# Kernel optimization log

Measured on AMD Instinct MI355X. Metric: run time of the kernel, lower is better.

## Reference

```python
import jax, jax.numpy as jnp
import numpy as np
from jax import lax

EPS = 1e-12

def _l2norm(x):
    # F.normalize(x, dim=-1): x / max(||x||, eps)
    n = jnp.sqrt(jnp.sum(x * x, axis=-1, keepdims=True))
    return x / jnp.maximum(n, EPS)

def _knn_edges(z, k):
    """k nearest neighbors (excluding self) via squared euclidean distance.
    Squared distance preserves the top-k ordering of torch.cdist."""
    N = z.shape[0]
    sq = jnp.sum(z * z, axis=1)                        # [N]
    d2 = sq[:, None] + sq[None, :] - 2.0 * (z @ z.T)   # [N, N]
    _, idx = lax.top_k(-d2, k + 1)                     # nearest first; col 0 is self
    tgt = idx[:, 1:].reshape(-1)                       # [N*k]
    src = jnp.repeat(jnp.arange(N, dtype=idx.dtype), k)
    return src, tgt

def _count_components(A):
    """Connected components on dense boolean adjacency A [N,N] via
    min-label propagation with pointer jumping (jit-friendly BFS replacement)."""
    N = A.shape[0]
    labels0 = jnp.arange(N, dtype=jnp.int32)

    def cond(state):
        return state[1]

    def body(state):
        labels, _ = state
        # min label over neighbors (N as sentinel where no edge)
        nbr_min = jnp.min(jnp.where(A, labels[None, :], jnp.int32(N)), axis=1)
        new = jnp.minimum(labels, nbr_min)
        new = new[new]  # pointer jumping: label of my label
        return new, jnp.any(new != labels)

    labels, _ = lax.while_loop(cond, body, (labels0, jnp.array(True)))
    # a node whose final label equals its own index is the component minimum
    return jnp.sum(labels == jnp.arange(N, dtype=jnp.int32))

def _level(feats, W, ratio):
    N = feats.shape[0]
    z = _l2norm(feats @ W.T)                 # Linear(bias=False) then normalize
    k = max(3, int(ratio * N))               # static python int
    k = min(k, N - 1)
    src, tgt = _knn_edges(z, k)
    A = jnp.zeros((N, N), dtype=bool)
    A = A.at[src, tgt].set(True).at[tgt, src].set(True)   # symmetrize
    comps = _count_components(lax.stop_gradient(A))
    num_edges = N * k                                     # src.numel() in torch code
    b0 = comps
    b1 = jnp.maximum(0, num_edges - N + comps)
    return b0, b1

RATIOS = (0.1, 0.05)

def setup_inputs() -> dict:
    key = jax.random.key(0)
    k1, k2, k3 = jax.random.split(key, 3)
    N, C = 4096, 512
    feats = jax.random.normal(k1, (N, C), dtype=jnp.float32)
    W0 = jax.random.normal(k2, (512, C), dtype=jnp.float32) / np.sqrt(C)
    W1 = jax.random.normal(k3, (256, C), dtype=jnp.float32) / np.sqrt(C)
    return {"feats": feats, "W0": W0, "W1": W1}

def reference(feats, W0, W1):
    b0_0, b1_0 = _level(feats, W0, RATIOS[0])
    b0_1, b1_1 = _level(feats, W1, RATIOS[1])
    return jnp.stack([b0_0 + b0_1, b1_0 + b1_1]).astype(jnp.float32)
```

## Files before the change

kernel.cpp:

```cpp
#include <hip/hip_runtime.h>
#include <hip/hip_bf16.h>

#define NPTS   4096
#define ADJ_W  128

typedef __attribute__((ext_vector_type(8))) short short8;
typedef __attribute__((ext_vector_type(8))) unsigned short u16x8;
typedef __attribute__((ext_vector_type(4))) unsigned short u16x4;
typedef __attribute__((ext_vector_type(16))) unsigned char u8x16;
typedef __attribute__((ext_vector_type(4))) float f32x4;
typedef __attribute__((ext_vector_type(4))) int i32x4;
typedef __attribute__((ext_vector_type(4))) unsigned u32x4;

__device__ __forceinline__ unsigned short bf16_bits(float x) {
  __hip_bfloat16 h = __float2bfloat16(x);
  return __builtin_bit_cast(unsigned short, h);
}

__device__ __forceinline__ unsigned char quant8(float f) {
  return (unsigned char)(int)fminf(fmaxf((f + 0.25f) * 512.0f, 0.0f), 255.0f);
}

__device__ __forceinline__ void async16(const void* g, void* l) {
  __builtin_amdgcn_global_load_lds(
      (const __attribute__((address_space(1))) void*)g,
      (__attribute__((address_space(3))) void*)l, 16, 0, 0);
}

__global__ __launch_bounds__(256) void convert_all(
    const float* __restrict__ feats, const float* __restrict__ W0,
    const float* __restrict__ W1, unsigned short* __restrict__ fh,
    unsigned short* __restrict__ wcat) {
  const int NF = 4096 * 512 / 4, NW0 = 512 * 512 / 4, NW1 = 256 * 512 / 4;
  for (int u = blockIdx.x * 256 + threadIdx.x; u < NF + NW0 + NW1;
       u += gridDim.x * 256) {
    const float* src;
    unsigned short* dst;
    int idx;
    if (u < NF)            { src = feats; dst = fh;   idx = u; }
    else if (u < NF + NW0) { src = W0;    dst = wcat; idx = u - NF; }
    else                   { src = W1;    dst = wcat + NW0 * 4; idx = u - NF - NW0; }
    f32x4 v = *(const f32x4*)(src + (size_t)idx * 4);
    u16x4 o;
    #pragma unroll
    for (int e = 0; e < 4; e++) o[e] = bf16_bits(v[e]);
    *(u16x4*)(dst + (size_t)idx * 4) = o;
  }
}

__global__ __launch_bounds__(256) void gemm_bt_f32(
    const __hip_bfloat16* __restrict__ A, const __hip_bfloat16* __restrict__ B,
    float* __restrict__ C, int M, int N, int K) {
  __shared__ __attribute__((aligned(16))) __hip_bfloat16 As[2][128 * 32];
  __shared__ __attribute__((aligned(16))) __hip_bfloat16 Bs[2][128 * 32];
  int tid = threadIdx.x;
  int lane = tid & 63, wave = tid >> 6;
  int wr = wave >> 1, wc = wave & 1;
  int row0 = blockIdx.y * 128, col0 = blockIdx.x * 128;

  f32x4 acc[4][4] = {};
  int r = lane & 15, kh = lane >> 4;

  auto stage = [&](int buf, int k0) {
    #pragma unroll
    for (int q = 0; q < 2; q++) {
      int chunk = q * 256 + tid;
      int row = chunk >> 2;
      int cb = chunk & 3;
      async16(&A[(size_t)(row0 + row) * K + k0 + cb * 8],
              &As[buf][(q * 256 + wave * 64) * 8]);
      async16(&B[(size_t)(col0 + row) * K + k0 + cb * 8],
              &Bs[buf][(q * 256 + wave * 64) * 8]);
    }
  };

  int nt = K >> 5;
  stage(0, 0);
  int cur = 0;
  for (int t = 0; t < nt; t++) {
    if (t + 1 < nt) {
      stage(cur ^ 1, (t + 1) * 32);
      asm volatile("s_waitcnt vmcnt(4)" ::: "memory");
    } else {
      asm volatile("s_waitcnt vmcnt(0)" ::: "memory");
    }
    __builtin_amdgcn_s_barrier();
    __builtin_amdgcn_sched_barrier(0);

    short8 a[4], b[4];
    #pragma unroll
    for (int mi = 0; mi < 4; mi++)
      a[mi] = *(short8*)(&As[cur][(wr * 64 + mi * 16 + r) * 32 + kh * 8]);
    #pragma unroll
    for (int ni = 0; ni < 4; ni++)
      b[ni] = *(short8*)(&Bs[cur][(wc * 64 + ni * 16 + r) * 32 + kh * 8]);
    #pragma unroll
    for (int mi = 0; mi < 4; mi++)
      #pragma unroll
      for (int ni = 0; ni < 4; ni++)
        acc[mi][ni] = __builtin_amdgcn_mfma_f32_16x16x32_bf16(a[mi], b[ni], acc[mi][ni], 0, 0, 0);
    __builtin_amdgcn_s_barrier();
    cur ^= 1;
  }

  int rq = lane >> 4;
  #pragma unroll
  for (int mi = 0; mi < 4; mi++)
    #pragma unroll
    for (int ni = 0; ni < 4; ni++)
      #pragma unroll
      for (int j = 0; j < 4; j++) {
        int rr = row0 + wr * 64 + mi * 16 + rq * 4 + j;
        int cc = col0 + wc * 64 + ni * 16 + r;
        C[(size_t)rr * N + cc] = acc[mi][ni][j];
      }
}

__global__ __launch_bounds__(512) void gemm_s_tri(
    const __hip_bfloat16* __restrict__ Z0, const __hip_bfloat16* __restrict__ Z1,
    unsigned char* __restrict__ S0, unsigned char* __restrict__ S1) {
  __shared__ __attribute__((aligned(16))) __hip_bfloat16 As[2][128 * 32];
  __shared__ __attribute__((aligned(16))) __hip_bfloat16 Bs[2][128 * 32];
  unsigned char* Cs = (unsigned char*)As;

  int b = blockIdx.x;
  int s = (b & 7) * 132 + (b >> 3);
  int lvl = s & 1;
  int t = s >> 1;
  int I = (int)((sqrtf(8.0f * (float)t + 1.0f) - 1.0f) * 0.5f);
  if (t - I * (I + 1) / 2 > I) I++;
  int J = t - I * (I + 1) / 2;

  const __hip_bfloat16* Z = lvl ? Z1 : Z0;
  unsigned char* S = lvl ? S1 : S0;
  int K = lvl ? 256 : 512;
  int row0 = I * 128, col0 = J * 128;

  int tid = threadIdx.x;
  int lane = tid & 63, wave = tid >> 6;
  int wr = wave >> 2, wc = wave & 3;

  f32x4 acc[4][2] = {};
  int r = lane & 15, kh = lane >> 4, rq = lane >> 4;

  auto stage = [&](int buf, int k0) {
    int row = tid >> 2;
    int cb = tid & 3;
    async16(&Z[(size_t)(row0 + row) * K + k0 + cb * 8],
            &As[buf][(wave * 64) * 8]);
    async16(&Z[(size_t)(col0 + row) * K + k0 + cb * 8],
            &Bs[buf][(wave * 64) * 8]);
  };

  int nt = K >> 5;
  stage(0, 0);
  int cur = 0;
  for (int tt = 0; tt < nt; tt++) {
    if (tt + 1 < nt) {
      stage(cur ^ 1, (tt + 1) * 32);
      asm volatile("s_waitcnt vmcnt(2)" ::: "memory");
    } else {
      asm volatile("s_waitcnt vmcnt(0)" ::: "memory");
    }
    __builtin_amdgcn_s_barrier();
    __builtin_amdgcn_sched_barrier(0);

    short8 a[4], bfr[2];
    #pragma unroll
    for (int mi = 0; mi < 4; mi++)
      a[mi] = *(short8*)(&As[cur][(wr * 64 + mi * 16 + r) * 32 + kh * 8]);
    #pragma unroll
    for (int ni = 0; ni < 2; ni++)
      bfr[ni] = *(short8*)(&Bs[cur][(wc * 32 + ni * 16 + r) * 32 + kh * 8]);
    #pragma unroll
    for (int mi = 0; mi < 4; mi++)
      #pragma unroll
      for (int ni = 0; ni < 2; ni++)
        acc[mi][ni] = __builtin_amdgcn_mfma_f32_16x16x32_bf16(a[mi], bfr[ni], acc[mi][ni], 0, 0, 0);
    __builtin_amdgcn_s_barrier();
    cur ^= 1;
  }
  __syncthreads();

  int erow = tid >> 4;
  int ecol = (tid & 15) * 8;

  #pragma unroll
  for (int s4 = 0; s4 < 4; s4++) {
    if (wr == (s4 >> 1)) {
      const int half = s4 & 1;
      #pragma unroll
      for (int mi_l = 0; mi_l < 2; mi_l++) {
        const int mi = half * 2 + mi_l;
        #pragma unroll
        for (int ni = 0; ni < 2; ni++) {
          int lrow0 = mi * 16 + rq * 4 - half * 32;
          int cc = wc * 32 + ni * 16 + r;
          #pragma unroll
          for (int j = 0; j < 4; j++)
            Cs[(lrow0 + j) * 144 + cc] = quant8(acc[mi][ni][j]);
        }
      }
    }
    __syncthreads();
    {
      unsigned long long v = *(const unsigned long long*)(&Cs[erow * 144 + ecol]);
      *(unsigned long long*)(&S[(size_t)(row0 + s4 * 32 + erow) * NPTS + col0 + ecol]) = v;
    }
    __syncthreads();
  }

  if (I != J) {
    #pragma unroll
    for (int s4 = 0; s4 < 4; s4++) {
      if (wc == s4) {
        #pragma unroll
        for (int ni = 0; ni < 2; ni++) {
          int lrow = ni * 16 + r;
          #pragma unroll
          for (int mi = 0; mi < 4; mi++) {
            int rr = wr * 64 + mi * 16 + rq * 4;
            unsigned v = (unsigned)quant8(acc[mi][ni][0])
                       | ((unsigned)quant8(acc[mi][ni][1]) << 8)
                       | ((unsigned)quant8(acc[mi][ni][2]) << 16)
                       | ((unsigned)quant8(acc[mi][ni][3]) << 24);
            *(unsigned*)(&Cs[lrow * 144 + rr]) = v;
          }
        }
      }
      __syncthreads();
      {
        unsigned long long v = *(const unsigned long long*)(&Cs[erow * 144 + ecol]);
        *(unsigned long long*)(&S[(size_t)(col0 + s4 * 32 + erow) * NPTS + row0 + ecol]) = v;
      }
      __syncthreads();
    }
  }
}

__global__ __launch_bounds__(64) void l2norm_fused(const float* __restrict__ Zcat,
                                                   unsigned short* __restrict__ Z0h,
                                                   unsigned short* __restrict__ Z1h) {
  int bid = blockIdx.x;
  int lvl = bid >> 12, row = bid & 4095;
  int D = lvl ? 256 : 512;
  const float* src = Zcat + (size_t)row * 768 + (lvl ? 512 : 0);
  unsigned short* dst = lvl ? (Z1h + (size_t)row * 256) : (Z0h + (size_t)row * 512);
  int d4 = D >> 2;
  int lane = threadIdx.x;
  float ss = 0.f;
  for (int j = lane; j < d4; j += 64) {
    f32x4 v = *(const f32x4*)(src + j * 4);
    ss += v[0] * v[0] + v[1] * v[1] + v[2] * v[2] + v[3] * v[3];
  }
  #pragma unroll
  for (int off = 32; off; off >>= 1) ss += __shfl_xor(ss, off);
  float inv = 1.0f / fmaxf(sqrtf(ss), 1e-12f);
  for (int j = lane; j < d4; j += 64) {
    f32x4 v = *(const f32x4*)(src + j * 4);
    u16x4 o;
    #pragma unroll
    for (int e = 0; e < 4; e++) o[e] = bf16_bits(v[e] * inv);
    *(u16x4*)(dst + j * 4) = o;
  }
}

__global__ __launch_bounds__(256) void select_mark_f(
    const unsigned char* __restrict__ S0, const unsigned char* __restrict__ S1,
    unsigned* __restrict__ adjR) {
  __shared__ int hist[4][256];
  __shared__ int sfx[257];
  __shared__ int wtot[4];
  __shared__ unsigned rowbits[ADJ_W];
  __shared__ int sh_b;
  int bid = blockIdx.x;
  int lvl = bid >> 12, i = bid & 4095;
  int k = lvl ? 204 : 409;
  const unsigned char* row = (lvl ? S1 : S0) + (size_t)i * NPTS;
  unsigned* adj = adjR + ((size_t)lvl * NPTS + i) * ADJ_W;
  int tid = threadIdx.x;
  int lane = tid & 63, wid = tid >> 6;
  int target = k + 1;

  #pragma unroll
  for (int w = 0; w < 4; w++) hist[w][tid] = 0;
  if (tid < ADJ_W) rowbits[tid] = 0;
  __syncthreads();

  u8x16 v = *(const u8x16*)(row + tid * 16);
  #pragma unroll
  for (int e = 0; e < 16; e++)
    atomicAdd(&hist[wid][v[e]], 1);
  __syncthreads();

  {
    int c = hist[0][tid] + hist[1][tid] + hist[2][tid] + hist[3][tid];
    int sv = c;
    #pragma unroll
    for (int off = 1; off < 64; off <<= 1) {
      int u = __shfl_down(sv, off);
      if (lane + off < 64) sv += u;
    }
    if (lane == 0) wtot[wid] = sv;
    __syncthreads();
    int add = 0;
    for (int w = wid + 1; w < 4; w++) add += wtot[w];
    sfx[tid] = sv + add;
    if (tid == 0) sfx[256] = 0;
  }
  __syncthreads();
  if (sfx[tid] >= target && sfx[tid + 1] < target) sh_b = tid;
  __syncthreads();
  int bq = sh_b;

  #pragma unroll
  for (int e = 0; e < 16; e++) {
    int j = tid * 16 + e;
    if ((int)v[e] >= bq) atomicOr(&rowbits[j >> 5], 1u << (j & 31));
  }
  __syncthreads();
  if (tid == 0) rowbits[i >> 5] &= ~(1u << (i & 31));
  __syncthreads();
  if (tid < ADJ_W) adj[tid] = rowbits[tid];
}

__global__ __launch_bounds__(256) void sym_or_f(const unsigned* __restrict__ adjR,
                                                unsigned* __restrict__ adjS) {
  int bid = blockIdx.x;
  int lvl = bid >> 11;
  size_t base = (size_t)lvl * NPTS * ADJ_W;
  int tid = threadIdx.x;
  int lane = tid & 63, wave = tid >> 6;
  int half = lane >> 5, l = lane & 31;
  int tile = (bid & 2047) * 8 + wave * 2 + half;
  int I = tile >> 7, J = tile & 127;
  unsigned y = adjR[base + (size_t)(J * 32 + l) * ADJ_W + I];
  #pragma unroll
  for (int j = 16; j; j >>= 1) {
    unsigned m = 0xFFFFFFFFu / ((1u << j) + 1u);
    unsigned t = __shfl_xor(y, j);
    y = ((l & j) == 0) ? ((y & m) | ((t & m) << j))
                       : ((y & ~m) | ((t >> j) & m));
  }
  size_t d = base + (size_t)(I * 32 + l) * ADJ_W + J;
  adjS[d] = adjR[d] | y;
}

__global__ __launch_bounds__(256) void sweep0_f(const unsigned* __restrict__ adjS,
                                                int* __restrict__ labels) {
  int gi = blockIdx.x * 256 + threadIdx.x;
  int lvl = gi >> 12, node = gi & 4095;
  const unsigned* row = adjS + ((size_t)lvl * NPTS + node) * ADJ_W;
  int m = node;
  for (int w = 0; w < ADJ_W; w += 4) {
    u32x4 v = *(const u32x4*)(row + w);
    if (v[0]) { m = min(m, (w + 0) * 32 + __ffs(v[0]) - 1); break; }
    if (v[1]) { m = min(m, (w + 1) * 32 + __ffs(v[1]) - 1); break; }
    if (v[2]) { m = min(m, (w + 2) * 32 + __ffs(v[2]) - 1); break; }
    if (v[3]) { m = min(m, (w + 3) * 32 + __ffs(v[3]) - 1); break; }
  }
  labels[gi] = m;
}

__global__ __launch_bounds__(128) void prop_f(const unsigned* __restrict__ adjS,
                                              int* __restrict__ labels) {
  __shared__ int L[NPTS];
  int bid = blockIdx.x;
  int lvl = bid >> 12, i = bid & 4095;
  const unsigned* adj = adjS + ((size_t)lvl * NPTS + i) * ADJ_W;
  int* lab = labels + (lvl << 12);
  for (int t = threadIdx.x * 4; t < NPTS; t += 128 * 4)
    *(i32x4*)&L[t] = *(const i32x4*)&lab[t];
  __syncthreads();
  int w = threadIdx.x;
  unsigned bits = adj[w];
  int base = w << 5;
  int m = 0x7FFFFFFF;
  while (bits) {
    int b = __ffs(bits) - 1;
    bits &= bits - 1;
    m = min(m, L[base + b]);
  }
  #pragma unroll
  for (int off = 32; off; off >>= 1) m = min(m, __shfl_down(m, off));
  __shared__ int s2[2];
  if ((w & 63) == 0) s2[w >> 6] = m;
  __syncthreads();
  if (w == 0) {
    int mm = min(min(s2[0], s2[1]), L[i]);
    mm = min(mm, lab[mm]);
    lab[i] = mm;
  }
}

__global__ __launch_bounds__(256) void finalize2(const int* __restrict__ labels,
                                                 float* __restrict__ out) {
  __shared__ int c[2];
  int tid = threadIdx.x;
  if (tid < 2) c[tid] = 0;
  __syncthreads();
  int c0 = 0, c1 = 0;
  for (int j = tid; j < NPTS; j += 256) {
    c0 += (labels[j] == j);
    c1 += (labels[NPTS + j] == j);
  }
  #pragma unroll
  for (int off = 32; off; off >>= 1) {
    c0 += __shfl_down(c0, off);
    c1 += __shfl_down(c1, off);
  }
  if ((tid & 63) == 0) {
    atomicAdd(&c[0], c0);
    atomicAdd(&c[1], c1);
  }
  __syncthreads();
  if (tid == 0) {
    float f0 = (float)c[0], f1 = (float)c[1];
    float ne0 = 4096.f * 409.f, ne1 = 4096.f * 204.f;
    out[0] = f0 + f1;
    out[1] = fmaxf(0.f, ne0 - 4096.f + f0) + fmaxf(0.f, ne1 - 4096.f + f1);
  }
}

extern "C" void kernel_launch(void* const* d_in, const int* in_sizes, int n_in,
                              void* d_out, int out_size, void* d_ws, size_t ws_size,
                              hipStream_t stream) {
  const float* feats = (const float*)d_in[0];
  const float* W0    = (const float*)d_in[1];
  const float* W1    = (const float*)d_in[2];
  float* out = (float*)d_out;

  char* ws = (char*)d_ws;
  unsigned char*  S0      = (unsigned char*)(ws);
  unsigned char*  S1      = (unsigned char*)(ws + (16ull << 20));
  float*          Zcat    = (float*)(ws + (32ull << 20));
  __hip_bfloat16* Z0h     = (__hip_bfloat16*)(ws + (44ull << 20));
  __hip_bfloat16* Z1h     = (__hip_bfloat16*)(ws + (48ull << 20));
  __hip_bfloat16* fh      = (__hip_bfloat16*)(ws + (50ull << 20));
  __hip_bfloat16* wcat    = (__hip_bfloat16*)(ws + (54ull << 20));
  unsigned*       adjR    = (unsigned*)(ws + (55ull << 20));
  unsigned*       adjS    = (unsigned*)(ws + (59ull << 20));
  int*            labels  = (int*)(ws + (63ull << 20));

  convert_all<<<2048, 256, 0, stream>>>(feats, W0, W1,
                                        (unsigned short*)fh, (unsigned short*)wcat);
  gemm_bt_f32<<<dim3(768 / 128, 4096 / 128), 256, 0, stream>>>(
      fh, wcat, Zcat, 4096, 768, 512);
  l2norm_fused<<<8192, 64, 0, stream>>>(Zcat, (unsigned short*)Z0h,
                                        (unsigned short*)Z1h);
  gemm_s_tri<<<1056, 512, 0, stream>>>(Z0h, Z1h, S0, S1);
  select_mark_f<<<2 * NPTS, 256, 0, stream>>>(S0, S1, adjR);
  sym_or_f<<<4096, 256, 0, stream>>>(adjR, adjS);
  sweep0_f<<<32, 256, 0, stream>>>(adjS, labels);
  prop_f<<<2 * NPTS, 128, 0, stream>>>(adjS, labels);
  prop_f<<<2 * NPTS, 128, 0, stream>>>(adjS, labels);
  finalize2<<<1, 256, 0, stream>>>(labels, out);
}
```

Before: 122.7 us.

## Fuse fp32-to-bf16 conversion into projection GEMM and triple-buffer similarity GEMM

Removes the separate convert kernel by having the projection GEMM load fp32 feats and weights directly, convert them to bf16 in registers and store them to LDS, with W0/W1 chosen per column block. This drops one launch and the round trip through bf16 staging buffers. In exchange the projection GEMM loses its async double-buffered prefetch and now does synchronous loads with two barriers per K step. Separately, the triangular similarity GEMM goes from two to three LDS buffers, prefetching two tiles ahead with adjusted vmcnt waits.

Measured after the change: 124.6 us. Within noise of the previous version (+1.5%).

```diff
diff --git a/kernel.cpp b/kernel.cpp
--- a/kernel.cpp
+++ b/kernel.cpp
@@ -27,80 +27,60 @@
       (__attribute__((address_space(3))) void*)l, 16, 0, 0);
 }
 
-__global__ __launch_bounds__(256) void convert_all(
+__global__ __launch_bounds__(256) void gemm_z_fused(
     const float* __restrict__ feats, const float* __restrict__ W0,
-    const float* __restrict__ W1, unsigned short* __restrict__ fh,
-    unsigned short* __restrict__ wcat) {
-  const int NF = 4096 * 512 / 4, NW0 = 512 * 512 / 4, NW1 = 256 * 512 / 4;
-  for (int u = blockIdx.x * 256 + threadIdx.x; u < NF + NW0 + NW1;
-       u += gridDim.x * 256) {
-    const float* src;
-    unsigned short* dst;
-    int idx;
-    if (u < NF)            { src = feats; dst = fh;   idx = u; }
-    else if (u < NF + NW0) { src = W0;    dst = wcat; idx = u - NF; }
-    else                   { src = W1;    dst = wcat + NW0 * 4; idx = u - NF - NW0; }
-    f32x4 v = *(const f32x4*)(src + (size_t)idx * 4);
-    u16x4 o;
-    #pragma unroll
-    for (int e = 0; e < 4; e++) o[e] = bf16_bits(v[e]);
-    *(u16x4*)(dst + (size_t)idx * 4) = o;
-  }
-}
-
-__global__ __launch_bounds__(256) void gemm_bt_f32(
-    const __hip_bfloat16* __restrict__ A, const __hip_bfloat16* __restrict__ B,
-    float* __restrict__ C, int M, int N, int K) {
-  __shared__ __attribute__((aligned(16))) __hip_bfloat16 As[2][128 * 32];
-  __shared__ __attribute__((aligned(16))) __hip_bfloat16 Bs[2][128 * 32];
+    const float* __restrict__ W1, float* __restrict__ C) {
+  __shared__ __attribute__((aligned(16))) __hip_bfloat16 As[128 * 32];
+  __shared__ __attribute__((aligned(16))) __hip_bfloat16 Bs[128 * 32];
+  const int K = 512, N = 768;
   int tid = threadIdx.x;
   int lane = tid & 63, wave = tid >> 6;
   int wr = wave >> 1, wc = wave & 1;
   int row0 = blockIdx.y * 128, col0 = blockIdx.x * 128;
+  const float* Bsrc = (col0 < 512) ? (W0 + (size_t)col0 * K)
+                                   : (W1 + (size_t)(col0 - 512) * K);
 
   f32x4 acc[4][4] = {};
   int r = lane & 15, kh = lane >> 4;
 
-  auto stage = [&](int buf, int k0) {
+  for (int k0 = 0; k0 < K; k0 += 32) {
     #pragma unroll
     for (int q = 0; q < 2; q++) {
       int chunk = q * 256 + tid;
       int row = chunk >> 2;
       int cb = chunk & 3;
-      async16(&A[(size_t)(row0 + row) * K + k0 + cb * 8],
-              &As[buf][(q * 256 + wave * 64) * 8]);
-      async16(&B[(size_t)(col0 + row) * K + k0 + cb * 8],
-              &Bs[buf][(q * 256 + wave * 64) * 8]);
-    }
-  };
-
-  int nt = K >> 5;
-  stage(0, 0);
-  int cur = 0;
-  for (int t = 0; t < nt; t++) {
-    if (t + 1 < nt) {
-      stage(cur ^ 1, (t + 1) * 32);
-      asm volatile("s_waitcnt vmcnt(4)" ::: "memory");
-    } else {
-      asm volatile("s_waitcnt vmcnt(0)" ::: "memory");
-    }
-    __builtin_amdgcn_s_barrier();
-    __builtin_amdgcn_sched_barrier(0);
+      const float* ap = feats + (size_t)(row0 + row) * K + k0 + cb * 8;
+      f32x4 a0 = *(const f32x4*)(ap);
+      f32x4 a1 = *(const f32x4*)(ap + 4);
+      const float* bp = Bsrc + (size_t)row * K + k0 + cb * 8;
+      f32x4 b0 = *(const f32x4*)(bp);
+      f32x4 b1 = *(const f32x4*)(bp + 4);
+      short8 av, bv;
+      #pragma unroll
+      for (int e = 0; e < 4; e++) {
+        av[e]     = (short)bf16_bits(a0[e]);
+        av[e + 4] = (short)bf16_bits(a1[e]);
+        bv[e]     = (short)bf16_bits(b0[e]);
+        bv[e + 4] = (short)bf16_bits(b1[e]);
+      }
+      *(short8*)(&As[chunk * 8]) = av;
+      *(short8*)(&Bs[chunk * 8]) = bv;
+    }
+    __syncthreads();
 
     short8 a[4], b[4];
     #pragma unroll
     for (int mi = 0; mi < 4; mi++)
-      a[mi] = *(short8*)(&As[cur][(wr * 64 + mi * 16 + r) * 32 + kh * 8]);
+      a[mi] = *(short8*)(&As[(wr * 64 + mi * 16 + r) * 32 + kh * 8]);
     #pragma unroll
     for (int ni = 0; ni < 4; ni++)
-      b[ni] = *(short8*)(&Bs[cur][(wc * 64 + ni * 16 + r) * 32 + kh * 8]);
+      b[ni] = *(short8*)(&Bs[(wc * 64 + ni * 16 + r) * 32 + kh * 8]);
     #pragma unroll
     for (int mi = 0; mi < 4; mi++)
       #pragma unroll
       for (int ni = 0; ni < 4; ni++)
         acc[mi][ni] = __builtin_amdgcn_mfma_f32_16x16x32_bf16(a[mi], b[ni], acc[mi][ni], 0, 0, 0);
-    __builtin_amdgcn_s_barrier();
-    cur ^= 1;
+    __syncthreads();
   }
 
   int rq = lane >> 4;
@@ -119,8 +99,8 @@
 __global__ __launch_bounds__(512) void gemm_s_tri(
     const __hip_bfloat16* __restrict__ Z0, const __hip_bfloat16* __restrict__ Z1,
     unsigned char* __restrict__ S0, unsigned char* __restrict__ S1) {
-  __shared__ __attribute__((aligned(16))) __hip_bfloat16 As[2][128 * 32];
-  __shared__ __attribute__((aligned(16))) __hip_bfloat16 Bs[2][128 * 32];
+  __shared__ __attribute__((aligned(16))) __hip_bfloat16 As[3][128 * 32];
+  __shared__ __attribute__((aligned(16))) __hip_bfloat16 Bs[3][128 * 32];
   unsigned char* Cs = (unsigned char*)As;
 
   int b = blockIdx.x;
@@ -154,10 +134,13 @@
 
   int nt = K >> 5;
   stage(0, 0);
-  int cur = 0;
+  stage(1, 32);
   for (int tt = 0; tt < nt; tt++) {
-    if (tt + 1 < nt) {
-      stage(cur ^ 1, (tt + 1) * 32);
+    int cur = tt % 3;
+    if (tt + 2 < nt) stage((tt + 2) % 3, (tt + 2) * 32);
+    if (tt + 3 <= nt) {
+      asm volatile("s_waitcnt vmcnt(4)" ::: "memory");
+    } else if (tt + 2 == nt) {
       asm volatile("s_waitcnt vmcnt(2)" ::: "memory");
     } else {
       asm volatile("s_waitcnt vmcnt(0)" ::: "memory");
@@ -178,7 +161,6 @@
       for (int ni = 0; ni < 2; ni++)
         acc[mi][ni] = __builtin_amdgcn_mfma_f32_16x16x32_bf16(a[mi], bfr[ni], acc[mi][ni], 0, 0, 0);
     __builtin_amdgcn_s_barrier();
-    cur ^= 1;
   }
   __syncthreads();
 
@@ -436,16 +418,12 @@
   float*          Zcat    = (float*)(ws + (32ull << 20));
   __hip_bfloat16* Z0h     = (__hip_bfloat16*)(ws + (44ull << 20));
   __hip_bfloat16* Z1h     = (__hip_bfloat16*)(ws + (48ull << 20));
-  __hip_bfloat16* fh      = (__hip_bfloat16*)(ws + (50ull << 20));
-  __hip_bfloat16* wcat    = (__hip_bfloat16*)(ws + (54ull << 20));
-  unsigned*       adjR    = (unsigned*)(ws + (55ull << 20));
-  unsigned*       adjS    = (unsigned*)(ws + (59ull << 20));
-  int*            labels  = (int*)(ws + (63ull << 20));
-
-  convert_all<<<2048, 256, 0, stream>>>(feats, W0, W1,
-                                        (unsigned short*)fh, (unsigned short*)wcat);
-  gemm_bt_f32<<<dim3(768 / 128, 4096 / 128), 256, 0, stream>>>(
-      fh, wcat, Zcat, 4096, 768, 512);
+  unsigned*       adjR    = (unsigned*)(ws + (50ull << 20));
+  unsigned*       adjS    = (unsigned*)(ws + (54ull << 20));
+  int*            labels  = (int*)(ws + (58ull << 20));
+
+  gemm_z_fused<<<dim3(768 / 128, 4096 / 128), 256, 0, stream>>>(
+      feats, W0, W1, Zcat);
   l2norm_fused<<<8192, 64, 0, stream>>>(Zcat, (unsigned short*)Z0h,
                                         (unsigned short*)Z1h);
   gemm_s_tri<<<1056, 512, 0, stream>>>(Z0h, Z1h, S0, S1);
```
